# Kernel tuning notes

Measured on AMD Instinct MI355X. Metric: run time of the kernel, lower is better.

The kernel has to match this reference:

```python
import jax, jax.numpy as jnp
import numpy as np

N_NODES, N_EDGES = 100000, 1000000
NODE_IN, EDGE_IN, D_MODEL = 128, 64, 128


def setup_inputs() -> dict:
    key = jax.random.key(0)
    k1, k2, k3, k4, k5 = jax.random.split(key, 5)
    x_node = jax.random.normal(k1, (N_NODES, NODE_IN), dtype=jnp.float32)
    x_edge = jax.random.normal(k2, (N_EDGES, EDGE_IN), dtype=jnp.float32)
    edge_index = jax.random.randint(k3, (2, N_EDGES), 0, N_NODES, dtype=jnp.int64)
    # learned params (PyTorch Linear: y = x @ W.T + b)
    s_e = 1.0 / np.sqrt(EDGE_IN)
    s_n = 1.0 / np.sqrt(NODE_IN)
    W_edge = jax.random.uniform(k4, (D_MODEL, EDGE_IN), jnp.float32, -s_e, s_e)
    b_edge = jnp.zeros((D_MODEL,), jnp.float32)
    W_node = jax.random.uniform(k5, (D_MODEL, NODE_IN), jnp.float32, -s_n, s_n)
    b_node = jnp.zeros((D_MODEL,), jnp.float32)
    ln_gamma = jnp.ones((D_MODEL,), jnp.float32)
    ln_beta = jnp.zeros((D_MODEL,), jnp.float32)
    return {
        "x_node": x_node, "x_edge": x_edge, "edge_index": edge_index,
        "W_edge": W_edge, "b_edge": b_edge,
        "W_node": W_node, "b_node": b_node,
        "ln_gamma": ln_gamma, "ln_beta": ln_beta,
    }


def _layernorm(x, gamma, beta, eps=1e-5):
    mu = jnp.mean(x, axis=-1, keepdims=True)
    var = jnp.mean(jnp.square(x - mu), axis=-1, keepdims=True)
    return (x - mu) * jax.lax.rsqrt(var + eps) * gamma + beta


def reference(x_node, x_edge, edge_index, W_edge, b_edge, W_node, b_node, ln_gamma, ln_beta):
    src, dst = edge_index[0], edge_index[1]
    h_edge = x_edge @ W_edge.T + b_edge                       # [E, D]
    h_node = x_node @ W_node.T + b_node                       # [N, D] project once, then gather
    h_endpoints = (h_node[src] + h_node[dst]) * 0.5           # [E, D]
    return _layernorm(h_edge + h_endpoints, ln_gamma, ln_beta)
```

## Files before the change

kernel.cpp:

```cpp
#include <hip/hip_runtime.h>


typedef __attribute__((ext_vector_type(8))) short bf16x8;
typedef __attribute__((ext_vector_type(4))) float f32x4;

__device__ __forceinline__ short f2bf(float f) {
  unsigned u = __float_as_uint(f);
  u = (u + 0x7FFFu + ((u >> 16) & 1u)) >> 16;
  return (short)u;
}
__device__ __forceinline__ float bf2f(short s) {
  return __uint_as_float(((unsigned)(unsigned short)s) << 16);
}
__device__ __forceinline__ bf16x8 cvt8(const float* __restrict__ p) {
  const f32x4 a = *(const f32x4*)p;
  const f32x4 b = *(const f32x4*)(p + 4);
  bf16x8 r;
  r[0] = f2bf(a[0]); r[1] = f2bf(a[1]); r[2] = f2bf(a[2]); r[3] = f2bf(a[3]);
  r[4] = f2bf(b[0]); r[5] = f2bf(b[1]); r[6] = f2bf(b[2]); r[7] = f2bf(b[3]);
  return r;
}

__global__ __launch_bounds__(256) void node_mfma_kernel(
    const float* __restrict__ x_node,
    const float* __restrict__ W_node,
    const float* __restrict__ b_node,
    short* __restrict__ h_node,
    int n_nodes)
{
  const int lane = threadIdx.x & 63;
  const int c = lane & 15, g = lane >> 4;
  const int gw = blockIdx.x * 4 + (threadIdx.x >> 6);
  const int nw = gridDim.x * 4;
  const int ntiles = (n_nodes + 15) >> 4;

  bf16x8 aW[8][4];
#pragma unroll
  for (int t = 0; t < 8; ++t)
#pragma unroll
    for (int s = 0; s < 4; ++s)
      aW[t][s] = cvt8(W_node + (size_t)(16 * t + c) * 128 + 32 * s + 8 * g);

  for (int tile = gw; tile < ntiles; tile += nw) {
    const int n0 = tile << 4;
    const int n = (n0 + c < n_nodes) ? n0 + c : n_nodes - 1;
    const float* xr = x_node + (size_t)n * 128;
    bf16x8 bx[4];
#pragma unroll
    for (int s = 0; s < 4; ++s) bx[s] = cvt8(xr + 32 * s + 8 * g);

    f32x4 acc[8];
#pragma unroll
    for (int t = 0; t < 8; ++t)
      acc[t] = *(const f32x4*)(b_node + 16 * t + 4 * g);
#pragma unroll
    for (int t = 0; t < 8; ++t)
#pragma unroll
      for (int s = 0; s < 4; ++s)
        acc[t] = __builtin_amdgcn_mfma_f32_16x16x32_bf16(aW[t][s], bx[s], acc[t], 0, 0, 0);

    if (n0 + c < n_nodes) {
      short* o = h_node + (size_t)(n0 + c) * 128 + g * 32;
#pragma unroll
      for (int k = 0; k < 4; ++k) {
        bf16x8 v;
#pragma unroll
        for (int j = 0; j < 4; ++j) {
          v[j]     = f2bf(acc[2 * k][j]);
          v[4 + j] = f2bf(acc[2 * k + 1][j]);
        }
        *(bf16x8*)(o + 8 * k) = v;
      }
    }
  }
}

__global__ __launch_bounds__(256) void edge_mfma_kernel(
    const float* __restrict__ x_edge,
    const int*   __restrict__ eidx,
    const float* __restrict__ W_edge,
    const float* __restrict__ b_edge,
    const short* __restrict__ h_node,
    const float* __restrict__ gamma,
    const float* __restrict__ beta,
    float* __restrict__ out,
    int n_edges)
{
  __shared__ short Wlds[8192];
  __shared__ float plds[384];

  const int tid = threadIdx.x;
  {
    const int r = tid >> 1, h = tid & 1;
    const float* wr = W_edge + (size_t)r * 64 + 32 * h;
#pragma unroll
    for (int q = 0; q < 4; ++q) {
      const bf16x8 v = cvt8(wr + 8 * q);
      const int slot = (4 * h + q) ^ (r & 7);
      *(bf16x8*)(&Wlds[r * 64 + slot * 8]) = v;
    }
    if (tid < 128) {
      plds[tid]       = b_edge[tid];
      plds[128 + tid] = gamma[tid];
      plds[256 + tid] = beta[tid];
    }
  }
  __syncthreads();

  const int lane = threadIdx.x & 63;
  const int c = lane & 15, g = lane >> 4;
  const int gw = blockIdx.x * 4 + (threadIdx.x >> 6);
  const int nw = gridDim.x * 4;
  const int ntiles = (n_edges + 15) >> 4;

  const int w0off = c * 64 + ((g) ^ (c & 7)) * 8;
  const int w1off = c * 64 + ((4 + g) ^ (c & 7)) * 8;

  if (gw >= ntiles) return;

  auto LOADIDX = [&](int tile, int& src, int& dst) {
    const int e = (tile * 16 + c < n_edges) ? tile * 16 + c : n_edges - 1;
    src = eidx[e];
    dst = eidx[n_edges + e];
  };
  auto LOADX = [&](int tile, bf16x8& b0, bf16x8& b1) {
    const int e = (tile * 16 + c < n_edges) ? tile * 16 + c : n_edges - 1;
    const float* xr = x_edge + (size_t)e * 64;
    b0 = cvt8(xr + 8 * g);
    b1 = cvt8(xr + 32 + 8 * g);
  };
  auto GATHER = [&](int src, int dst, bf16x8* vs, bf16x8* vd) {
    const short* hs = h_node + (size_t)src * 128 + g * 32;
    const short* hd = h_node + (size_t)dst * 128 + g * 32;
#pragma unroll
    for (int k = 0; k < 4; ++k) {
      vs[k] = *(const bf16x8*)(hs + 8 * k);
      vd[k] = *(const bf16x8*)(hd + 8 * k);
    }
  };
  auto COMPUTE = [&](int tile, bf16x8 b0, bf16x8 b1, bf16x8* vs, bf16x8* vd) {
    f32x4 acc[8];
#pragma unroll
    for (int k = 0; k < 4; ++k)
#pragma unroll
      for (int j = 0; j < 4; ++j) {
        acc[2 * k][j]     = plds[16 * (2 * k) + 4 * g + j]
                          + 0.5f * (bf2f(vs[k][j]) + bf2f(vd[k][j]));
        acc[2 * k + 1][j] = plds[16 * (2 * k + 1) + 4 * g + j]
                          + 0.5f * (bf2f(vs[k][4 + j]) + bf2f(vd[k][4 + j]));
      }
#pragma unroll
    for (int t = 0; t < 8; ++t) {
      const bf16x8 a0 = *(const bf16x8*)(&Wlds[t * 1024 + w0off]);
      const bf16x8 a1 = *(const bf16x8*)(&Wlds[t * 1024 + w1off]);
      acc[t] = __builtin_amdgcn_mfma_f32_16x16x32_bf16(a0, b0, acc[t], 0, 0, 0);
      acc[t] = __builtin_amdgcn_mfma_f32_16x16x32_bf16(a1, b1, acc[t], 0, 0, 0);
    }
    float s1 = 0.f;
#pragma unroll
    for (int t = 0; t < 8; ++t)
      s1 += (acc[t][0] + acc[t][1]) + (acc[t][2] + acc[t][3]);
    s1 += __shfl_xor(s1, 16, 64);
    s1 += __shfl_xor(s1, 32, 64);
    const float mu = s1 * (1.f / 128.f);

    float s2 = 0.f;
#pragma unroll
    for (int t = 0; t < 8; ++t)
#pragma unroll
      for (int j = 0; j < 4; ++j) {
        const float d = acc[t][j] - mu;
        acc[t][j] = d;
        s2 = fmaf(d, d, s2);
      }
    s2 += __shfl_xor(s2, 16, 64);
    s2 += __shfl_xor(s2, 32, 64);
    const float rstd = rsqrtf(s2 * (1.f / 128.f) + 1e-5f);

    if (tile * 16 + c < n_edges) {
      float* o = out + (size_t)(tile * 16 + c) * 128 + 4 * g;
#pragma unroll
      for (int t = 0; t < 8; ++t) {
        f32x4 r;
#pragma unroll
        for (int j = 0; j < 4; ++j)
          r[j] = fmaf(acc[t][j] * rstd, plds[128 + 16 * t + 4 * g + j],
                      plds[256 + 16 * t + 4 * g + j]);
        *(f32x4*)(o + 16 * t) = r;
      }
    }
  };

  bf16x8 bxA0, bxA1, bxB0, bxB1;
  bf16x8 vsA[4], vdA[4], vsB[4], vdB[4];
  int srcA, dstA, srcB, dstB;

  LOADIDX(gw, srcA, dstA);
  LOADX(gw, bxA0, bxA1);
  GATHER(srcA, dstA, vsA, vdA);
  LOADIDX(gw + nw, srcB, dstB);
  LOADX(gw + nw, bxB0, bxB1);

  int t = gw;
  for (;;) {
    GATHER(srcB, dstB, vsB, vdB);
    LOADIDX(t + 2 * nw, srcA, dstA);
    COMPUTE(t, bxA0, bxA1, vsA, vdA);
    LOADX(t + 2 * nw, bxA0, bxA1);
    t += nw;
    if (t >= ntiles) break;

    GATHER(srcA, dstA, vsA, vdA);
    LOADIDX(t + 2 * nw, srcB, dstB);
    COMPUTE(t, bxB0, bxB1, vsB, vdB);
    LOADX(t + 2 * nw, bxB0, bxB1);
    t += nw;
    if (t >= ntiles) break;
  }
}

extern "C" void kernel_launch(void* const* d_in, const int* in_sizes, int n_in,
                              void* d_out, int out_size, void* d_ws, size_t ws_size,
                              hipStream_t stream) {
  const float* x_node = (const float*)d_in[0];
  const float* x_edge = (const float*)d_in[1];
  const int*   eidx   = (const int*)  d_in[2];
  const float* W_edge = (const float*)d_in[3];
  const float* b_edge = (const float*)d_in[4];
  const float* W_node = (const float*)d_in[5];
  const float* b_node = (const float*)d_in[6];
  const float* gamma  = (const float*)d_in[7];
  const float* beta   = (const float*)d_in[8];
  float* out = (float*)d_out;

  const int n_nodes = in_sizes[0] / 128;
  const int n_edges = in_sizes[2] / 2;

  short* h_node = (short*)d_ws;
  if (ws_size < (size_t)n_nodes * 128 * sizeof(short)) return;

  node_mfma_kernel<<<512, 256, 0, stream>>>(x_node, W_node, b_node, h_node, n_nodes);
  edge_mfma_kernel<<<2048, 256, 0, stream>>>(x_edge, eidx, W_edge, b_edge,
                                             h_node, gamma, beta, out, n_edges);
}
```

Baseline: 275.8 us.

## Move node weights to LDS and shrink edge pipeline for higher occupancy

The node projection kernel now stages W_node as bf16 in swizzled shared memory instead of holding 32 bf16x8 fragments per lane in registers, and reads the bias from LDS. The edge kernel drops its double-buffered A/B software pipeline for a single-buffer loop. In that loop the next tile's gathers are issued right after the current gathered values are consumed into the accumulators, so the gather latency overlaps the MFMA and layernorm work. Both kernels get a launch-bounds minimum of 5 blocks per CU so the compiler caps register use. The goal is more resident waves to hide the random h_node gather latency, at the cost of a shallower prefetch distance and extra LDS reads in the node kernel.

```diff
diff --git a/kernel.cpp b/kernel.cpp
--- a/kernel.cpp
+++ b/kernel.cpp
@@ -21,25 +21,39 @@
   return r;
 }
 
-__global__ __launch_bounds__(256) void node_mfma_kernel(
+__global__ __launch_bounds__(256, 5) void node_mfma_kernel(
     const float* __restrict__ x_node,
     const float* __restrict__ W_node,
     const float* __restrict__ b_node,
     short* __restrict__ h_node,
     int n_nodes)
 {
-  const int lane = threadIdx.x & 63;
+  __shared__ short Wlds[16384];
+  __shared__ float blds[128];
+
+  const int tid = threadIdx.x;
+  {
+    const int r = tid >> 1, h = tid & 1;
+    const float* wr = W_node + (size_t)r * 128 + 64 * h;
+#pragma unroll
+    for (int q = 0; q < 8; ++q) {
+      const bf16x8 v = cvt8(wr + 8 * q);
+      const int slot = (8 * h + q) ^ (r & 7);
+      *(bf16x8*)(&Wlds[r * 128 + slot * 8]) = v;
+    }
+    if (tid < 128) blds[tid] = b_node[tid];
+  }
+  __syncthreads();
+
+  const int lane = tid & 63;
   const int c = lane & 15, g = lane >> 4;
-  const int gw = blockIdx.x * 4 + (threadIdx.x >> 6);
+  const int gw = blockIdx.x * 4 + (tid >> 6);
   const int nw = gridDim.x * 4;
   const int ntiles = (n_nodes + 15) >> 4;
 
-  bf16x8 aW[8][4];
-#pragma unroll
-  for (int t = 0; t < 8; ++t)
-#pragma unroll
-    for (int s = 0; s < 4; ++s)
-      aW[t][s] = cvt8(W_node + (size_t)(16 * t + c) * 128 + 32 * s + 8 * g);
+  int woff[4];
+#pragma unroll
+  for (int s = 0; s < 4; ++s) woff[s] = c * 128 + ((4 * s + g) ^ (c & 7)) * 8;
 
   for (int tile = gw; tile < ntiles; tile += nw) {
     const int n0 = tile << 4;
@@ -52,12 +66,14 @@
     f32x4 acc[8];
 #pragma unroll
     for (int t = 0; t < 8; ++t)
-      acc[t] = *(const f32x4*)(b_node + 16 * t + 4 * g);
+      acc[t] = *(const f32x4*)(blds + 16 * t + 4 * g);
 #pragma unroll
     for (int t = 0; t < 8; ++t)
 #pragma unroll
-      for (int s = 0; s < 4; ++s)
-        acc[t] = __builtin_amdgcn_mfma_f32_16x16x32_bf16(aW[t][s], bx[s], acc[t], 0, 0, 0);
+      for (int s = 0; s < 4; ++s) {
+        const bf16x8 a = *(const bf16x8*)(&Wlds[t * 2048 + woff[s]]);
+        acc[t] = __builtin_amdgcn_mfma_f32_16x16x32_bf16(a, bx[s], acc[t], 0, 0, 0);
+      }
 
     if (n0 + c < n_nodes) {
       short* o = h_node + (size_t)(n0 + c) * 128 + g * 32;
@@ -75,7 +91,7 @@
   }
 }
 
-__global__ __launch_bounds__(256) void edge_mfma_kernel(
+__global__ __launch_bounds__(256, 5) void edge_mfma_kernel(
     const float* __restrict__ x_edge,
     const int*   __restrict__ eidx,
     const float* __restrict__ W_edge,
@@ -107,9 +123,9 @@
   }
   __syncthreads();
 
-  const int lane = threadIdx.x & 63;
+  const int lane = tid & 63;
   const int c = lane & 15, g = lane >> 4;
-  const int gw = blockIdx.x * 4 + (threadIdx.x >> 6);
+  const int gw = blockIdx.x * 4 + (tid >> 6);
   const int nw = gridDim.x * 4;
   const int ntiles = (n_edges + 15) >> 4;
 
@@ -138,7 +154,20 @@
       vd[k] = *(const bf16x8*)(hd + 8 * k);
     }
   };
-  auto COMPUTE = [&](int tile, bf16x8 b0, bf16x8 b1, bf16x8* vs, bf16x8* vd) {
+
+  bf16x8 bx0, bx1, bxN0, bxN1;
+  bf16x8 vs[4], vd[4];
+  int srcN, dstN;
+
+  {
+    int src0, dst0;
+    LOADIDX(gw, src0, dst0);
+    LOADX(gw, bx0, bx1);
+    GATHER(src0, dst0, vs, vd);
+    LOADIDX(gw + nw, srcN, dstN);
+  }
+
+  for (int t = gw; t < ntiles; t += nw) {
     f32x4 acc[8];
 #pragma unroll
     for (int k = 0; k < 4; ++k)
@@ -149,73 +178,54 @@
         acc[2 * k + 1][j] = plds[16 * (2 * k + 1) + 4 * g + j]
                           + 0.5f * (bf2f(vs[k][4 + j]) + bf2f(vd[k][4 + j]));
       }
-#pragma unroll
-    for (int t = 0; t < 8; ++t) {
-      const bf16x8 a0 = *(const bf16x8*)(&Wlds[t * 1024 + w0off]);
-      const bf16x8 a1 = *(const bf16x8*)(&Wlds[t * 1024 + w1off]);
-      acc[t] = __builtin_amdgcn_mfma_f32_16x16x32_bf16(a0, b0, acc[t], 0, 0, 0);
-      acc[t] = __builtin_amdgcn_mfma_f32_16x16x32_bf16(a1, b1, acc[t], 0, 0, 0);
-    }
+
+    GATHER(srcN, dstN, vs, vd);
+    LOADIDX(t + 2 * nw, srcN, dstN);
+    LOADX(t + nw, bxN0, bxN1);
+
+#pragma unroll
+    for (int tt = 0; tt < 8; ++tt) {
+      const bf16x8 a0 = *(const bf16x8*)(&Wlds[tt * 1024 + w0off]);
+      const bf16x8 a1 = *(const bf16x8*)(&Wlds[tt * 1024 + w1off]);
+      acc[tt] = __builtin_amdgcn_mfma_f32_16x16x32_bf16(a0, bx0, acc[tt], 0, 0, 0);
+      acc[tt] = __builtin_amdgcn_mfma_f32_16x16x32_bf16(a1, bx1, acc[tt], 0, 0, 0);
+    }
+
     float s1 = 0.f;
 #pragma unroll
-    for (int t = 0; t < 8; ++t)
-      s1 += (acc[t][0] + acc[t][1]) + (acc[t][2] + acc[t][3]);
+    for (int tt = 0; tt < 8; ++tt)
+      s1 += (acc[tt][0] + acc[tt][1]) + (acc[tt][2] + acc[tt][3]);
     s1 += __shfl_xor(s1, 16, 64);
     s1 += __shfl_xor(s1, 32, 64);
     const float mu = s1 * (1.f / 128.f);
 
     float s2 = 0.f;
 #pragma unroll
-    for (int t = 0; t < 8; ++t)
+    for (int tt = 0; tt < 8; ++tt)
 #pragma unroll
       for (int j = 0; j < 4; ++j) {
-        const float d = acc[t][j] - mu;
-        acc[t][j] = d;
+        const float d = acc[tt][j] - mu;
+        acc[tt][j] = d;
         s2 = fmaf(d, d, s2);
       }
     s2 += __shfl_xor(s2, 16, 64);
     s2 += __shfl_xor(s2, 32, 64);
     const float rstd = rsqrtf(s2 * (1.f / 128.f) + 1e-5f);
 
-    if (tile * 16 + c < n_edges) {
-      float* o = out + (size_t)(tile * 16 + c) * 128 + 4 * g;
-#pragma unroll
-      for (int t = 0; t < 8; ++t) {
+    if (t * 16 + c < n_edges) {
+      float* o = out + (size_t)(t * 16 + c) * 128 + 4 * g;
+#pragma unroll
+      for (int tt = 0; tt < 8; ++tt) {
         f32x4 r;
 #pragma unroll
         for (int j = 0; j < 4; ++j)
-          r[j] = fmaf(acc[t][j] * rstd, plds[128 + 16 * t + 4 * g + j],
-                      plds[256 + 16 * t + 4 * g + j]);
-        *(f32x4*)(o + 16 * t) = r;
-      }
-    }
-  };
-
-  bf16x8 bxA0, bxA1, bxB0, bxB1;
-  bf16x8 vsA[4], vdA[4], vsB[4], vdB[4];
-  int srcA, dstA, srcB, dstB;
-
-  LOADIDX(gw, srcA, dstA);
-  LOADX(gw, bxA0, bxA1);
-  GATHER(srcA, dstA, vsA, vdA);
-  LOADIDX(gw + nw, srcB, dstB);
-  LOADX(gw + nw, bxB0, bxB1);
-
-  int t = gw;
-  for (;;) {
-    GATHER(srcB, dstB, vsB, vdB);
-    LOADIDX(t + 2 * nw, srcA, dstA);
-    COMPUTE(t, bxA0, bxA1, vsA, vdA);
-    LOADX(t + 2 * nw, bxA0, bxA1);
-    t += nw;
-    if (t >= ntiles) break;
-
-    GATHER(srcA, dstA, vsA, vdA);
-    LOADIDX(t + 2 * nw, srcB, dstB);
-    COMPUTE(t, bxB0, bxB1, vsB, vdB);
-    LOADX(t + 2 * nw, bxB0, bxB1);
-    t += nw;
-    if (t >= ntiles) break;
+          r[j] = fmaf(acc[tt][j] * rstd, plds[128 + 16 * tt + 4 * g + j],
+                      plds[256 + 16 * tt + 4 * g + j]);
+        *(f32x4*)(o + 16 * tt) = r;
+      }
+    }
+
+    bx0 = bxN0; bx1 = bxN1;
   }
 }
 
```

After: 562.0 us. 2.04x slower.
